# Kernel optimization log

Hardware: AMD Instinct MI355X
Metric: run time of the kernel (lower is better)

## Reference

```python
import jax, jax.numpy as jnp
import numpy as np

NUM_NODES = 50000
NUM_EDGES = 800000
NUM_GRAPHS = 64
EMBED = 128
HIDDEN = 128
LAYERS = 3
CLUSTERS = 16
OUT_DIM = 128
MAX_DEG = 64
EPS = 1e-5


def setup_inputs() -> dict:
    key = jax.random.key(0)
    ks = jax.random.split(key, 16)
    deg_idx = jax.random.randint(ks[0], (NUM_NODES,), 0, MAX_DEG + 1)
    edge_index = jax.random.randint(ks[1], (2, NUM_EDGES), 0, NUM_NODES)
    batch = jnp.sort(jax.random.randint(ks[2], (NUM_NODES,), 0, NUM_GRAPHS))
    s = 0.05
    emb = jax.random.normal(ks[3], (MAX_DEG + 1, EMBED), jnp.float32) * s
    Wl = jax.random.normal(ks[4], (LAYERS, HIDDEN, HIDDEN), jnp.float32) * s
    bl = jnp.zeros((LAYERS, HIDDEN), jnp.float32)
    Wr = jax.random.normal(ks[5], (LAYERS, HIDDEN, HIDDEN), jnp.float32) * s
    gamma = jnp.ones((LAYERS, HIDDEN), jnp.float32)
    beta = jnp.zeros((LAYERS, HIDDEN), jnp.float32)
    attn_W = jax.random.normal(ks[6], (HIDDEN, CLUSTERS), jnp.float32) * s
    attn_b = jnp.zeros((CLUSTERS,), jnp.float32)
    out_W = jax.random.normal(ks[7], (HIDDEN, OUT_DIM), jnp.float32) * s
    out_b = jnp.zeros((OUT_DIM,), jnp.float32)
    return {"emb": emb, "Wl": Wl, "bl": bl, "Wr": Wr, "gamma": gamma,
            "beta": beta, "attn_W": attn_W, "attn_b": attn_b,
            "out_W": out_W, "out_b": out_b, "deg_idx": deg_idx,
            "edge_index": edge_index, "batch": batch}


def reference(emb, Wl, bl, Wr, gamma, beta, attn_W, attn_b, out_W, out_b,
              deg_idx, edge_index, batch):
    N = deg_idx.shape[0]
    src, dst = edge_index[0], edge_index[1]
    x = emb[deg_idx]  # [N, EMBED]
    for l in range(Wl.shape[0]):
        # SAGEConv (mean aggr): lin_l(mean_j x_j) + lin_r(x); lin_r has no bias
        msg_sum = jax.ops.segment_sum(x[src], dst, num_segments=N)
        cnt = jax.ops.segment_sum(jnp.ones((src.shape[0], 1), x.dtype), dst,
                                  num_segments=N)
        mean = msg_sum / jnp.maximum(cnt, 1.0)
        x = mean @ Wl[l] + bl[l] + x @ Wr[l]
        # BatchNorm1d (training-mode batch stats, biased variance)
        mu = x.mean(axis=0)
        var = jnp.mean((x - mu) ** 2, axis=0)
        x = (x - mu) * jax.lax.rsqrt(var + EPS) * gamma[l] + beta[l]
        x = jax.nn.relu(x)  # dropout is identity in eval
    scores = x @ attn_W + attn_b  # [N, C] (num_heads == 1 -> squeeze)
    # per-graph softmax over nodes (segment softmax along dim 0)
    smax = jax.ops.segment_max(scores, batch, num_segments=NUM_GRAPHS)
    e = jnp.exp(scores - smax[batch])
    denom = jax.ops.segment_sum(e, batch, num_segments=NUM_GRAPHS)
    w = e / denom[batch]  # [N, C]
    # c_b = w_b^T @ x_b  -> segment-weighted sums: [B, C, H]
    clust = jax.ops.segment_sum(w[:, :, None] * x[:, None, :], batch,
                                num_segments=NUM_GRAPHS)
    return clust @ out_W + out_b  # [B, C, OUT_DIM]
```

## Files before the change

kernel.cpp:

```cpp
#include <hip/hip_runtime.h>

typedef unsigned short u16;
typedef unsigned int   u32;

#define H    128
#define C    16
#define ODIM 128

typedef short bf16x8 __attribute__((ext_vector_type(8)));
typedef float f32x4  __attribute__((ext_vector_type(4)));

#define WSP 272

__device__ __forceinline__ float bf2f(u32 v){
  union { u32 i; float f; } t; t.i = v << 16; return t.f;
}
__device__ __forceinline__ u16 f2bf(float f){
  u32 u = __float_as_uint(f);
  u32 r = u + 0x7fffu + ((u >> 16) & 1u);
  return (u16)(r >> 16);
}
__device__ __forceinline__ u32 pack2(float a, float b){
  return (u32)f2bf(a) | ((u32)f2bf(b) << 16);
}

__global__ __launch_bounds__(256) void k_embed(const float* __restrict__ emb,
    const int* __restrict__ deg, u16* __restrict__ xb, int N){
  int i = blockIdx.x*256 + threadIdx.x;
  if (i >= N*32) return;
  int n = i >> 5, q = i & 31;
  int d = deg[n];
  float4 v = ((const float4*)(emb + (size_t)d*H))[q];
  uint2 o; o.x = pack2(v.x, v.y); o.y = pack2(v.z, v.w);
  ((uint2*)(xb + (size_t)n*H))[q] = o;
}

__global__ __launch_bounds__(256) void k_bounds(const int* __restrict__ batch,
    int* __restrict__ gs, int N, int B){
  int n = blockIdx.x*256 + threadIdx.x;
  if (n >= N) return;
  int b = batch[n];
  if (n == 0){ for (int g = 0; g <= b; g++) gs[g] = 0; }
  else {
    int pb = batch[n-1];
    for (int g = pb+1; g <= b; g++) gs[g] = n;
  }
  if (n == N-1){ for (int g = b+1; g <= B; g++) gs[g] = N; }
}

__global__ __launch_bounds__(256) void k_wprep(const float* __restrict__ Wl,
    const float* __restrict__ Wr, u16* __restrict__ Wt){
  __shared__ u16 T[128][18];
  int b = blockIdx.x;
  int strip = b & 7, half = (b >> 3) & 1, l = b >> 4;
  const float* M = (half ? Wr : Wl) + (size_t)l*H*H;
  int k0 = strip * 16;
  int tid = threadIdx.x;
  #pragma unroll
  for (int j = 0; j < 8; j++){
    int u = tid + j*256;
    int kk = u >> 7, h = u & 127;
    T[h][kk] = f2bf(M[(size_t)(k0 + kk)*H + h]);
  }
  __syncthreads();
  #pragma unroll
  for (int j = 0; j < 8; j++){
    int u = tid + j*256;
    int h = u >> 4, k16 = u & 15;
    Wt[((size_t)(l*H + h))*256 + half*128 + k0 + k16] = T[h][k16];
  }
}


__global__ __launch_bounds__(256) void k_hist(const int* __restrict__ ei,
    int* __restrict__ blkhist, int NB, int E, int chunk){
  __shared__ int hist[400];
  int blk = blockIdx.x, tid = threadIdx.x;
  for (int b = tid; b < NB; b += 256) hist[b] = 0;
  __syncthreads();
  int start = blk*chunk, end = min(E, start + chunk);
  for (int e = start + tid; e < end; e += 256)
    atomicAdd(&hist[ei[E + e] >> 7], 1);
  __syncthreads();
  for (int b = tid; b < NB; b += 256) blkhist[b*64 + blk] = hist[b];
}

__global__ __launch_bounds__(256) void k_scanA(const int* __restrict__ in,
    int* __restrict__ out, int* __restrict__ bsum, int n){
  __shared__ int wsum[4];
  int tid = threadIdx.x;
  int base = blockIdx.x*1024 + tid*4;
  int v0 = (base+0 < n) ? in[base+0] : 0;
  int v1 = (base+1 < n) ? in[base+1] : 0;
  int v2 = (base+2 < n) ? in[base+2] : 0;
  int v3 = (base+3 < n) ? in[base+3] : 0;
  int tsum = v0+v1+v2+v3;
  int lane = tid & 63, w = tid >> 6;
  int incl = tsum;
  for (int d = 1; d < 64; d <<= 1){
    int t = __shfl_up(incl, d, 64);
    if (lane >= d) incl += t;
  }
  if (lane == 63) wsum[w] = incl;
  __syncthreads();
  int woff = 0;
  for (int i = 0; i < w; i++) woff += wsum[i];
  int excl = woff + incl - tsum;
  if (base+0 < n) out[base+0] = excl;
  if (base+1 < n) out[base+1] = excl + v0;
  if (base+2 < n) out[base+2] = excl + v0 + v1;
  if (base+3 < n) out[base+3] = excl + v0 + v1 + v2;
  if (tid == 255) bsum[blockIdx.x] = woff + incl;
}

__global__ __launch_bounds__(64) void k_scanB(const int* __restrict__ bsum,
    int* __restrict__ boff, int nb){
  int tid = threadIdx.x;
  int v = (tid < nb) ? bsum[tid] : 0;
  int incl = v;
  for (int d = 1; d < 64; d <<= 1){
    int t = __shfl_up(incl, d, 64);
    if (tid >= d) incl += t;
  }
  boff[tid] = incl - v;
}

__global__ __launch_bounds__(256) void k_scanC(int* __restrict__ out,
    const int* __restrict__ boff, int n){
  int i = blockIdx.x*256 + threadIdx.x;
  if (i < n) out[i] += boff[i >> 10];
}

__global__ __launch_bounds__(256) void k_place(const int* __restrict__ ei,
    const int* __restrict__ bases, int2* __restrict__ pairs,
    int NB, int E, int chunk){
  __shared__ int cursor[400];
  int blk = blockIdx.x, tid = threadIdx.x;
  for (int b = tid; b < NB; b += 256) cursor[b] = bases[b*64 + blk];
  __syncthreads();
  int start = blk*chunk, end = min(E, start + chunk);
  for (int e = start + tid; e < end; e += 256){
    int s = ei[e], d = ei[E + e];
    int pos = atomicAdd(&cursor[d >> 7], 1);
    pairs[pos] = make_int2(s, d);
  }
}

__global__ __launch_bounds__(256) void k_cnt_place(const int2* __restrict__ pairs,
    const int* __restrict__ bases, int* __restrict__ rowptr,
    int* __restrict__ col, int NB, int N, int E){
  int b = blockIdx.x, tid = threadIdx.x;
  int bstart = bases[b*64];
  int bend   = (b+1 < NB) ? bases[(b+1)*64] : E;
  __shared__ int cnt[128], sc[128], rank[128];
  if (tid < 128) cnt[tid] = 0;
  __syncthreads();
  for (int e = bstart + tid; e < bend; e += 256)
    atomicAdd(&cnt[pairs[e].y & 127], 1);
  __syncthreads();
  if (tid < 128) sc[tid] = cnt[tid];
  for (int d = 1; d < 128; d <<= 1){
    int v = 0;
    __syncthreads();
    if (tid < 128 && tid >= d) v = sc[tid - d];
    __syncthreads();
    if (tid < 128) sc[tid] += v;
  }
  __syncthreads();
  if (tid < 128){
    int excl = sc[tid] - cnt[tid];
    rank[tid] = bstart + excl;
    int node = b*128 + tid;
    if (node < N) rowptr[node] = bstart + excl;
  }
  if (b == NB-1 && tid == 0) rowptr[N] = E;
  __syncthreads();
  for (int e = bstart + tid; e < bend; e += 256){
    int2 p = pairs[e];
    int pos = atomicAdd(&rank[p.y & 127], 1);
    col[pos] = p.x;
  }
}

__global__ __launch_bounds__(256) void k_agg(const u16* __restrict__ x,
    const int* __restrict__ rowptr, const int* __restrict__ col,
    u16* __restrict__ meanb, int N){
  int wid  = (blockIdx.x*256 + threadIdx.x) >> 6;
  int lane = threadIdx.x & 63;
  if (wid >= N) return;
  int r0 = rowptr[wid], r1 = rowptr[wid+1];
  int grp = lane >> 4, fl = lane & 15;
  const u16* xf = x + fl*8;
  float a0=0.f,a1=0.f,a2=0.f,a3=0.f,a4=0.f,a5=0.f,a6=0.f,a7=0.f;
  for (int e = r0 + grp; e < r1; e += 4){
    int s = col[e];
    uint4 v = *(const uint4*)(xf + (size_t)s*H);
    a0 += bf2f(v.x & 0xffff); a1 += bf2f(v.x >> 16);
    a2 += bf2f(v.y & 0xffff); a3 += bf2f(v.y >> 16);
    a4 += bf2f(v.z & 0xffff); a5 += bf2f(v.z >> 16);
    a6 += bf2f(v.w & 0xffff); a7 += bf2f(v.w >> 16);
  }
  a0 += __shfl_xor(a0,16,64); a1 += __shfl_xor(a1,16,64);
  a2 += __shfl_xor(a2,16,64); a3 += __shfl_xor(a3,16,64);
  a4 += __shfl_xor(a4,16,64); a5 += __shfl_xor(a5,16,64);
  a6 += __shfl_xor(a6,16,64); a7 += __shfl_xor(a7,16,64);
  a0 += __shfl_xor(a0,32,64); a1 += __shfl_xor(a1,32,64);
  a2 += __shfl_xor(a2,32,64); a3 += __shfl_xor(a3,32,64);
  a4 += __shfl_xor(a4,32,64); a5 += __shfl_xor(a5,32,64);
  a6 += __shfl_xor(a6,32,64); a7 += __shfl_xor(a7,32,64);
  if (grp == 0){
    float invc = 1.0f / (float)max(r1 - r0, 1);
    uint4 o;
    o.x = pack2(a0*invc, a1*invc);
    o.y = pack2(a2*invc, a3*invc);
    o.z = pack2(a4*invc, a5*invc);
    o.w = pack2(a6*invc, a7*invc);
    *(uint4*)(meanb + (size_t)wid*H + fl*8) = o;
  }
}

__global__ __launch_bounds__(256) void k_linear(const u16* __restrict__ meanb,
    const u16* __restrict__ xb, const u16* __restrict__ Wt,
    const float* __restrict__ bl, float* __restrict__ x2,
    float* __restrict__ pstats, int N){
  __shared__ u16 Ws[128][WSP];
  __shared__ float Sh[128], Qh[128];
  int tid = threadIdx.x;
  if (tid < 128){ Sh[tid] = 0.f; Qh[tid] = 0.f; }
  int lane = tid & 63, w = tid >> 6;
  int mlane = lane & 15, quad = lane >> 4;
  int node = blockIdx.x*64 + w*16 + mlane;
  const u16* arow_m = meanb + (size_t)node*H + quad*8;
  const u16* arow_x = xb   + (size_t)node*H + quad*8;
  bf16x8 af[8];
  #pragma unroll
  for (int kk = 0; kk < 4; kk++){
    af[kk]     = *(const bf16x8*)(arow_m + kk*32);
    af[kk + 4] = *(const bf16x8*)(arow_x + kk*32);
  }
  #pragma unroll
  for (int j = 0; j < 16; j++){
    int u = tid + j*256;
    int row = u >> 5, seg = u & 31;
    uint4 v = ((const uint4*)(Wt + (size_t)row*256))[seg];
    *(uint4*)&Ws[row][seg*8] = v;
  }
  __syncthreads();
  f32x4 acc[8];
  #pragma unroll
  for (int t = 0; t < 8; t++) acc[t] = (f32x4){0.f, 0.f, 0.f, 0.f};
  #pragma unroll
  for (int kk = 0; kk < 8; kk++){
    #pragma unroll
    for (int t = 0; t < 8; t++){
      bf16x8 b = *(const bf16x8*)&Ws[t*16 + mlane][kk*32 + quad*8];
      acc[t] = __builtin_amdgcn_mfma_f32_16x16x32_bf16(af[kk], b, acc[t], 0, 0, 0);
    }
  }
  #pragma unroll
  for (int t = 0; t < 8; t++){
    int h = t*16 + mlane;
    float bv = bl[h];
    float s = 0.f, q = 0.f;
    #pragma unroll
    for (int r = 0; r < 4; r++){
      int nd = blockIdx.x*64 + w*16 + quad*4 + r;
      if (nd < N){
        float v = acc[t][r] + bv;
        x2[(size_t)nd*H + h] = v;
        s += v; q = fmaf(v, v, q);
      }
    }
    s += __shfl_xor(s, 16, 64); s += __shfl_xor(s, 32, 64);
    q += __shfl_xor(q, 16, 64); q += __shfl_xor(q, 32, 64);
    if (quad == 0){
      atomicAdd(&Sh[h], s);
      atomicAdd(&Qh[h], q);
    }
  }
  __syncthreads();
  {
    float v = (tid < 128) ? Sh[tid] : Qh[tid - 128];
    pstats[(size_t)blockIdx.x*256 + tid] = v;
  }
}

__global__ __launch_bounds__(256) void k_statred(const float* __restrict__ pstats,
    float* __restrict__ stats, int nblk){
  __shared__ float red[4];
  int c = blockIdx.x, tid = threadIdx.x;
  float s = 0.f;
  for (int b = tid; b < nblk; b += 256)
    s += pstats[(size_t)b*256 + c];
  s += __shfl_xor(s, 1, 64);  s += __shfl_xor(s, 2, 64);
  s += __shfl_xor(s, 4, 64);  s += __shfl_xor(s, 8, 64);
  s += __shfl_xor(s, 16, 64); s += __shfl_xor(s, 32, 64);
  if ((tid & 63) == 0) red[tid >> 6] = s;
  __syncthreads();
  if (tid == 0) stats[c] = red[0] + red[1] + red[2] + red[3];
}

__global__ __launch_bounds__(256) void k_bnrelu(const float* __restrict__ x2,
    const float* __restrict__ stats, const float* __restrict__ gamma,
    const float* __restrict__ beta, u16* __restrict__ xb, int N, float invN){
  int i = blockIdx.x*256 + threadIdx.x;
  if (i >= N*32) return;
  int h = (i & 31) * 4;
  float4 v = ((const float4*)x2)[i];
  float vv[4] = {v.x, v.y, v.z, v.w};
  float r[4];
  #pragma unroll
  for (int j = 0; j < 4; j++){
    float mu  = stats[h+j] * invN;
    float var = fmaf(-mu, mu, stats[H + h + j] * invN);
    float sc  = rsqrtf(var + 1e-5f) * gamma[h+j];
    float bi  = beta[h+j];
    r[j] = fmaxf(fmaf(vv[j] - mu, sc, bi), 0.0f);
  }
  uint2 o; o.x = pack2(r[0], r[1]); o.y = pack2(r[2], r[3]);
  ((uint2*)xb)[i] = o;
}

__global__ __launch_bounds__(256) void k_scores(const u16* __restrict__ xb,
    const float* __restrict__ attn_W, const float* __restrict__ attn_b,
    float* __restrict__ escore, int N){
  __shared__ float xs[64][133];
  __shared__ float aw[H*C];
  int tid = threadIdx.x;
  int n0 = blockIdx.x * 64;
  #pragma unroll
  for (int j = 0; j < 8; j++){
    int u = tid + j*256;
    aw[u] = attn_W[u];
  }
  #pragma unroll
  for (int j = 0; j < 4; j++){
    int u = tid + j*256;
    int row = u & 63, seg = u >> 6;
    int node = n0 + row;
    uint4 rv = make_uint4(0,0,0,0);
    if (node < N) rv = ((const uint4*)(xb + (size_t)node*H))[seg];
    int k = seg*8;
    xs[row][k+0]=bf2f(rv.x&0xffff); xs[row][k+1]=bf2f(rv.x>>16);
    xs[row][k+2]=bf2f(rv.y&0xffff); xs[row][k+3]=bf2f(rv.y>>16);
    xs[row][k+4]=bf2f(rv.z&0xffff); xs[row][k+5]=bf2f(rv.z>>16);
    xs[row][k+6]=bf2f(rv.w&0xffff); xs[row][k+7]=bf2f(rv.w>>16);
  }
  __syncthreads();
  int c = tid & 15, sub = tid >> 4;
  float bias = attn_b[c];
  float acc[4] = {bias, bias, bias, bias};
  for (int k = 0; k < H; k++){
    float w = aw[k*C + c];
    acc[0] = fmaf(xs[sub     ][k], w, acc[0]);
    acc[1] = fmaf(xs[sub + 16][k], w, acc[1]);
    acc[2] = fmaf(xs[sub + 32][k], w, acc[2]);
    acc[3] = fmaf(xs[sub + 48][k], w, acc[3]);
  }
  #pragma unroll
  for (int j = 0; j < 4; j++){
    int node = n0 + sub + 16*j;
    if (node < N) escore[(size_t)node*C + c] = __expf(acc[j]);
  }
}

__global__ __launch_bounds__(256) void k_denom(const float* __restrict__ escore,
    const int* __restrict__ gs, float* __restrict__ gsum){
  int g = blockIdx.x;
  int c = threadIdx.x & 15, sub = threadIdx.x >> 4;
  int a = gs[g], b = gs[g+1];
  float s = 0.f;
  for (int n = a + sub; n < b; n += 16) s += escore[(size_t)n*C + c];
  __shared__ float part[16][17];
  part[sub][c] = s;
  for (int off2 = 8; off2 > 0; off2 >>= 1){
    __syncthreads();
    if (sub < off2) part[sub][c] += part[sub + off2][c];
  }
  __syncthreads();
  if (threadIdx.x < C) gsum[(size_t)g*C + threadIdx.x] = part[0][threadIdx.x];
}

__global__ __launch_bounds__(256) void k_clust(const u16* __restrict__ xb,
    const float* __restrict__ escore, const int* __restrict__ gs,
    float* __restrict__ partial){
  int g = blockIdx.x >> 4, b = blockIdx.x & 15;
  int h = threadIdx.x & 127, cg = threadIdx.x >> 7;
  int a = gs[g], e2 = gs[g+1];
  float acc[8] = {0,0,0,0,0,0,0,0};
  for (int n = a + b; n < e2; n += 16){
    float xv = bf2f(xb[(size_t)n*H + h]);
    const float4* ep = (const float4*)(escore + (size_t)n*C) + cg*2;
    float4 e0 = ep[0], e1 = ep[1];
    acc[0] = fmaf(e0.x, xv, acc[0]);
    acc[1] = fmaf(e0.y, xv, acc[1]);
    acc[2] = fmaf(e0.z, xv, acc[2]);
    acc[3] = fmaf(e0.w, xv, acc[3]);
    acc[4] = fmaf(e1.x, xv, acc[4]);
    acc[5] = fmaf(e1.y, xv, acc[5]);
    acc[6] = fmaf(e1.z, xv, acc[6]);
    acc[7] = fmaf(e1.w, xv, acc[7]);
  }
  int c0 = cg*8;
  float* dst = partial + (((size_t)(g*16 + b))*C)*H + h;
  #pragma unroll
  for (int r = 0; r < 8; r++)
    dst[(size_t)(c0 + r)*H] = acc[r];
}

__global__ __launch_bounds__(256) void k_out(const float* __restrict__ partial,
    const float* __restrict__ gsum, const float* __restrict__ out_W,
    const float* __restrict__ out_b, float* __restrict__ out){
  __shared__ float cs[2][128];
  int tid = threadIdx.x;
  int r = tid >> 7, h = tid & 127;
  int row = blockIdx.x*2 + r;
  int g = row >> 4, c = row & 15;
  float s = 0.f;
  for (int b = 0; b < 16; b++)
    s += partial[(((size_t)(g*16 + b))*C + c)*H + h];
  cs[r][h] = s;
  __syncthreads();
  float gden = gsum[row];
  float inv = gden > 0.f ? 1.0f / gden : 0.f;
  float acc = 0.f;
  for (int hh = 0; hh < H; hh++)
    acc = fmaf(cs[r][hh], out_W[hh*ODIM + h], acc);
  out[(size_t)row*ODIM + h] = fmaf(acc, inv, out_b[h]);
}

extern "C" void kernel_launch(void* const* d_in, const int* in_sizes, int n_in,
                              void* d_out, int out_size, void* d_ws, size_t ws_size,
                              hipStream_t stream){
  const float* emb    = (const float*)d_in[0];
  const float* Wl     = (const float*)d_in[1];
  const float* bl     = (const float*)d_in[2];
  const float* Wr     = (const float*)d_in[3];
  const float* gamma  = (const float*)d_in[4];
  const float* beta   = (const float*)d_in[5];
  const float* attn_W = (const float*)d_in[6];
  const float* attn_b = (const float*)d_in[7];
  const float* out_W  = (const float*)d_in[8];
  const float* out_b  = (const float*)d_in[9];
  const int* deg    = (const int*)d_in[10];
  const int* ei     = (const int*)d_in[11];
  const int* batch  = (const int*)d_in[12];
  float* out = (float*)d_out;

  const int N = in_sizes[10];
  const int E = in_sizes[11] / 2;
  const int L = in_sizes[1] / (H*H);
  const int B = out_size / (C*ODIM);
  const int NB = (N + 127) >> 7;
  const int n25 = NB * 64;
  const int chunk = (E + 63) >> 6;
  const int nblkL = (N + 63) / 64;

  size_t off = 0;
  auto alloc = [&](size_t bytes) -> void* {
    void* p = (char*)d_ws + off;
    off += (bytes + 255) & ~(size_t)255;
    return p;
  };
  u16*   xb     = (u16*)  alloc((size_t)N*H*2);
  u16*   meanb  = (u16*)  alloc((size_t)N*H*2);
  float* x2     = (float*)alloc((size_t)N*H*4);
  int2*  pairs  = (int2*)x2;
  float* partial= x2;
  u16*   Wt     = (u16*)  alloc((size_t)L*H*256*2);
  float* escore = (float*)alloc((size_t)N*C*4);
  int*   col    = (int*)  alloc((size_t)E*4);
  int*   rowptr = (int*)  alloc((size_t)(N+1)*4);
  int*   blkhist= (int*)  alloc((size_t)n25*4);
  int*   bases  = (int*)  alloc((size_t)n25*4);
  int*   bsum   = (int*)  alloc(64*4);
  int*   boff   = (int*)  alloc(64*4);
  int*   gs     = (int*)  alloc((size_t)(B+1)*4);
  float* gsum   = (float*)alloc((size_t)B*C*4);
  float* stats  = (float*)alloc((size_t)L*2*H*4);
  float* pstats = (float*)alloc((size_t)nblkL*256*4);

  hipLaunchKernelGGL(k_embed,  dim3((N*32+255)/256), dim3(256), 0, stream, emb, deg, xb, N);
  hipLaunchKernelGGL(k_bounds, dim3((N+255)/256),    dim3(256), 0, stream, batch, gs, N, B);
  hipLaunchKernelGGL(k_wprep,  dim3(L*16),           dim3(256), 0, stream, Wl, Wr, Wt);
  hipLaunchKernelGGL(k_hist,   dim3(64),  dim3(256), 0, stream, ei, blkhist, NB, E, chunk);
  int nblk25 = (n25 + 1023) / 1024;
  hipLaunchKernelGGL(k_scanA,  dim3(nblk25), dim3(256), 0, stream, blkhist, bases, bsum, n25);
  hipLaunchKernelGGL(k_scanB,  dim3(1),      dim3(64),  0, stream, bsum, boff, nblk25);
  hipLaunchKernelGGL(k_scanC,  dim3((n25+255)/256), dim3(256), 0, stream, bases, boff, n25);
  hipLaunchKernelGGL(k_place,  dim3(64),  dim3(256), 0, stream, ei, bases, pairs, NB, E, chunk);
  hipLaunchKernelGGL(k_cnt_place, dim3(NB), dim3(256), 0, stream, pairs, bases, rowptr, col, NB, N, E);

  float invN = 1.0f / (float)N;
  for (int l = 0; l < L; l++){
    hipLaunchKernelGGL(k_agg,    dim3((N+3)/4),  dim3(256), 0, stream, xb, rowptr, col, meanb, N);
    hipLaunchKernelGGL(k_linear, dim3(nblkL),    dim3(256), 0, stream,
                       meanb, xb, Wt + (size_t)l*H*256, bl + (size_t)l*H, x2,
                       pstats, N);
    hipLaunchKernelGGL(k_statred,dim3(256),      dim3(256), 0, stream, pstats, stats + l*2*H, nblkL);
    hipLaunchKernelGGL(k_bnrelu, dim3((N*32+255)/256), dim3(256), 0, stream,
                       x2, stats + l*2*H, gamma + (size_t)l*H, beta + (size_t)l*H, xb, N, invN);
  }
  hipLaunchKernelGGL(k_scores, dim3((N+63)/64), dim3(256), 0, stream, xb, attn_W, attn_b, escore, N);
  hipLaunchKernelGGL(k_denom,  dim3(B),         dim3(256), 0, stream, escore, gs, gsum);
  hipLaunchKernelGGL(k_clust,  dim3(B*16),      dim3(256), 0, stream, xb, escore, gs, partial);
  hipLaunchKernelGGL(k_out,    dim3(B*C/2),     dim3(256), 0, stream, partial, gsum, out_W, out_b, out);
}
```

Baseline: 396.4 us.

## Fuse setup kernels, widen edge binning, unroll gather, fuse scores into BN

Merges the embed, graph-bounds, weight-prep and histogram kernels into a single block-partitioned setup launch. The edge binning now uses 256 chunks instead of 64 for more parallelism, with the scan widened to match. The aggregation loop is unrolled by two to keep more gathers in flight. The attention score computation is folded into the final BN/ReLU pass so the last-layer activations are not re-read. Together these cut launch count and memory traffic, at the cost of a larger histogram and extra shared memory and a block-wide barrier in the BN kernel.

```diff
diff --git a/kernel.cpp b/kernel.cpp
--- a/kernel.cpp
+++ b/kernel.cpp
@@ -11,6 +11,7 @@
 typedef float f32x4  __attribute__((ext_vector_type(4)));
 
 #define WSP 272
+#define NP  256
 
 __device__ __forceinline__ float bf2f(u32 v){
   union { u32 i; float f; } t; t.i = v << 16; return t.f;
@@ -24,65 +25,65 @@
   return (u32)f2bf(a) | ((u32)f2bf(b) << 16);
 }
 
-__global__ __launch_bounds__(256) void k_embed(const float* __restrict__ emb,
-    const int* __restrict__ deg, u16* __restrict__ xb, int N){
-  int i = blockIdx.x*256 + threadIdx.x;
-  if (i >= N*32) return;
-  int n = i >> 5, q = i & 31;
-  int d = deg[n];
-  float4 v = ((const float4*)(emb + (size_t)d*H))[q];
-  uint2 o; o.x = pack2(v.x, v.y); o.y = pack2(v.z, v.w);
-  ((uint2*)(xb + (size_t)n*H))[q] = o;
-}
-
-__global__ __launch_bounds__(256) void k_bounds(const int* __restrict__ batch,
-    int* __restrict__ gs, int N, int B){
-  int n = blockIdx.x*256 + threadIdx.x;
-  if (n >= N) return;
-  int b = batch[n];
-  if (n == 0){ for (int g = 0; g <= b; g++) gs[g] = 0; }
-  else {
-    int pb = batch[n-1];
-    for (int g = pb+1; g <= b; g++) gs[g] = n;
-  }
-  if (n == N-1){ for (int g = b+1; g <= B; g++) gs[g] = N; }
-}
-
-__global__ __launch_bounds__(256) void k_wprep(const float* __restrict__ Wl,
-    const float* __restrict__ Wr, u16* __restrict__ Wt){
-  __shared__ u16 T[128][18];
-  int b = blockIdx.x;
-  int strip = b & 7, half = (b >> 3) & 1, l = b >> 4;
-  const float* M = (half ? Wr : Wl) + (size_t)l*H*H;
-  int k0 = strip * 16;
-  int tid = threadIdx.x;
-  #pragma unroll
-  for (int j = 0; j < 8; j++){
-    int u = tid + j*256;
-    int kk = u >> 7, h = u & 127;
-    T[h][kk] = f2bf(M[(size_t)(k0 + kk)*H + h]);
-  }
-  __syncthreads();
-  #pragma unroll
-  for (int j = 0; j < 8; j++){
-    int u = tid + j*256;
-    int h = u >> 4, k16 = u & 15;
-    Wt[((size_t)(l*H + h))*256 + half*128 + k0 + k16] = T[h][k16];
-  }
-}
-
-
-__global__ __launch_bounds__(256) void k_hist(const int* __restrict__ ei,
-    int* __restrict__ blkhist, int NB, int E, int chunk){
-  __shared__ int hist[400];
-  int blk = blockIdx.x, tid = threadIdx.x;
-  for (int b = tid; b < NB; b += 256) hist[b] = 0;
-  __syncthreads();
-  int start = blk*chunk, end = min(E, start + chunk);
-  for (int e = start + tid; e < end; e += 256)
-    atomicAdd(&hist[ei[E + e] >> 7], 1);
-  __syncthreads();
-  for (int b = tid; b < NB; b += 256) blkhist[b*64 + blk] = hist[b];
+__global__ __launch_bounds__(256) void k_setup(const float* __restrict__ emb,
+    const int* __restrict__ deg, u16* __restrict__ xb,
+    const int* __restrict__ batch, int* __restrict__ gs,
+    const float* __restrict__ Wl, const float* __restrict__ Wr,
+    u16* __restrict__ Wt, const int* __restrict__ ei,
+    int* __restrict__ blkhist, int N, int B, int NB, int E, int chunk,
+    int g0, int g1, int g2){
+  __shared__ __align__(16) char smem[4608];
+  int bid = blockIdx.x, tid = threadIdx.x;
+  if (bid < g0){
+    int i = bid*256 + tid;
+    if (i < N*32){
+      int n = i >> 5, q = i & 31;
+      int d = deg[n];
+      float4 v = ((const float4*)(emb + (size_t)d*H))[q];
+      uint2 o; o.x = pack2(v.x, v.y); o.y = pack2(v.z, v.w);
+      ((uint2*)(xb + (size_t)n*H))[q] = o;
+    }
+  } else if (bid < g1){
+    int n = (bid - g0)*256 + tid;
+    if (n < N){
+      int b = batch[n];
+      if (n == 0){ for (int g = 0; g <= b; g++) gs[g] = 0; }
+      else {
+        int pb = batch[n-1];
+        for (int g = pb+1; g <= b; g++) gs[g] = n;
+      }
+      if (n == N-1){ for (int g = b+1; g <= B; g++) gs[g] = N; }
+    }
+  } else if (bid < g2){
+    u16 (*T)[18] = (u16(*)[18])smem;
+    int b = bid - g1;
+    int strip = b & 7, half = (b >> 3) & 1, l = b >> 4;
+    const float* M = (half ? Wr : Wl) + (size_t)l*H*H;
+    int k0 = strip * 16;
+    #pragma unroll
+    for (int j = 0; j < 8; j++){
+      int u = tid + j*256;
+      int kk = u >> 7, h = u & 127;
+      T[h][kk] = f2bf(M[(size_t)(k0 + kk)*H + h]);
+    }
+    __syncthreads();
+    #pragma unroll
+    for (int j = 0; j < 8; j++){
+      int u = tid + j*256;
+      int h = u >> 4, k16 = u & 15;
+      Wt[((size_t)(l*H + h))*256 + half*128 + k0 + k16] = T[h][k16];
+    }
+  } else {
+    int* hist = (int*)smem;
+    int blk = bid - g2;
+    for (int b = tid; b < NB; b += 256) hist[b] = 0;
+    __syncthreads();
+    int start = blk*chunk, end = min(E, start + chunk);
+    for (int e = start + tid; e < end; e += 256)
+      atomicAdd(&hist[ei[E + e] >> 7], 1);
+    __syncthreads();
+    for (int b = tid; b < NB; b += 256) blkhist[b*NP + blk] = hist[b];
+  }
 }
 
 __global__ __launch_bounds__(256) void k_scanA(const int* __restrict__ in,
@@ -113,16 +114,22 @@
   if (tid == 255) bsum[blockIdx.x] = woff + incl;
 }
 
-__global__ __launch_bounds__(64) void k_scanB(const int* __restrict__ bsum,
+__global__ __launch_bounds__(256) void k_scanB(const int* __restrict__ bsum,
     int* __restrict__ boff, int nb){
+  __shared__ int ws[4];
   int tid = threadIdx.x;
   int v = (tid < nb) ? bsum[tid] : 0;
+  int lane = tid & 63, w = tid >> 6;
   int incl = v;
   for (int d = 1; d < 64; d <<= 1){
     int t = __shfl_up(incl, d, 64);
-    if (tid >= d) incl += t;
-  }
-  boff[tid] = incl - v;
+    if (lane >= d) incl += t;
+  }
+  if (lane == 63) ws[w] = incl;
+  __syncthreads();
+  int woff = 0;
+  for (int i = 0; i < w; i++) woff += ws[i];
+  boff[tid] = woff + incl - v;
 }
 
 __global__ __launch_bounds__(256) void k_scanC(int* __restrict__ out,
@@ -136,7 +143,7 @@
     int NB, int E, int chunk){
   __shared__ int cursor[400];
   int blk = blockIdx.x, tid = threadIdx.x;
-  for (int b = tid; b < NB; b += 256) cursor[b] = bases[b*64 + blk];
+  for (int b = tid; b < NB; b += 256) cursor[b] = bases[b*NP + blk];
   __syncthreads();
   int start = blk*chunk, end = min(E, start + chunk);
   for (int e = start + tid; e < end; e += 256){
@@ -150,8 +157,8 @@
     const int* __restrict__ bases, int* __restrict__ rowptr,
     int* __restrict__ col, int NB, int N, int E){
   int b = blockIdx.x, tid = threadIdx.x;
-  int bstart = bases[b*64];
-  int bend   = (b+1 < NB) ? bases[(b+1)*64] : E;
+  int bstart = bases[b*NP];
+  int bend   = (b+1 < NB) ? bases[(b+1)*NP] : E;
   __shared__ int cnt[128], sc[128], rank[128];
   if (tid < 128) cnt[tid] = 0;
   __syncthreads();
@@ -192,9 +199,22 @@
   int grp = lane >> 4, fl = lane & 15;
   const u16* xf = x + fl*8;
   float a0=0.f,a1=0.f,a2=0.f,a3=0.f,a4=0.f,a5=0.f,a6=0.f,a7=0.f;
-  for (int e = r0 + grp; e < r1; e += 4){
-    int s = col[e];
-    uint4 v = *(const uint4*)(xf + (size_t)s*H);
+  int e = r0 + grp;
+  for (; e + 4 < r1; e += 8){
+    int s0 = col[e], s1 = col[e+4];
+    uint4 v = *(const uint4*)(xf + (size_t)s0*H);
+    uint4 u = *(const uint4*)(xf + (size_t)s1*H);
+    a0 += bf2f(v.x & 0xffff) + bf2f(u.x & 0xffff);
+    a1 += bf2f(v.x >> 16)    + bf2f(u.x >> 16);
+    a2 += bf2f(v.y & 0xffff) + bf2f(u.y & 0xffff);
+    a3 += bf2f(v.y >> 16)    + bf2f(u.y >> 16);
+    a4 += bf2f(v.z & 0xffff) + bf2f(u.z & 0xffff);
+    a5 += bf2f(v.z >> 16)    + bf2f(u.z >> 16);
+    a6 += bf2f(v.w & 0xffff) + bf2f(u.w & 0xffff);
+    a7 += bf2f(v.w >> 16)    + bf2f(u.w >> 16);
+  }
+  if (e < r1){
+    uint4 v = *(const uint4*)(xf + (size_t)col[e]*H);
     a0 += bf2f(v.x & 0xffff); a1 += bf2f(v.x >> 16);
     a2 += bf2f(v.y & 0xffff); a3 += bf2f(v.y >> 16);
     a4 += bf2f(v.z & 0xffff); a5 += bf2f(v.z >> 16);
@@ -302,65 +322,51 @@
 
 __global__ __launch_bounds__(256) void k_bnrelu(const float* __restrict__ x2,
     const float* __restrict__ stats, const float* __restrict__ gamma,
-    const float* __restrict__ beta, u16* __restrict__ xb, int N, float invN){
-  int i = blockIdx.x*256 + threadIdx.x;
-  if (i >= N*32) return;
-  int h = (i & 31) * 4;
-  float4 v = ((const float4*)x2)[i];
-  float vv[4] = {v.x, v.y, v.z, v.w};
-  float r[4];
-  #pragma unroll
-  for (int j = 0; j < 4; j++){
-    float mu  = stats[h+j] * invN;
-    float var = fmaf(-mu, mu, stats[H + h + j] * invN);
-    float sc  = rsqrtf(var + 1e-5f) * gamma[h+j];
-    float bi  = beta[h+j];
-    r[j] = fmaxf(fmaf(vv[j] - mu, sc, bi), 0.0f);
-  }
-  uint2 o; o.x = pack2(r[0], r[1]); o.y = pack2(r[2], r[3]);
-  ((uint2*)xb)[i] = o;
-}
-
-__global__ __launch_bounds__(256) void k_scores(const u16* __restrict__ xb,
+    const float* __restrict__ beta, u16* __restrict__ xb, int N, float invN,
     const float* __restrict__ attn_W, const float* __restrict__ attn_b,
-    float* __restrict__ escore, int N){
-  __shared__ float xs[64][133];
+    float* __restrict__ escore, int do_scores){
+  __shared__ float xs[8][132];
   __shared__ float aw[H*C];
+  __shared__ float ab[C];
   int tid = threadIdx.x;
-  int n0 = blockIdx.x * 64;
-  #pragma unroll
-  for (int j = 0; j < 8; j++){
-    int u = tid + j*256;
-    aw[u] = attn_W[u];
-  }
-  #pragma unroll
-  for (int j = 0; j < 4; j++){
-    int u = tid + j*256;
-    int row = u & 63, seg = u >> 6;
-    int node = n0 + row;
-    uint4 rv = make_uint4(0,0,0,0);
-    if (node < N) rv = ((const uint4*)(xb + (size_t)node*H))[seg];
-    int k = seg*8;
-    xs[row][k+0]=bf2f(rv.x&0xffff); xs[row][k+1]=bf2f(rv.x>>16);
-    xs[row][k+2]=bf2f(rv.y&0xffff); xs[row][k+3]=bf2f(rv.y>>16);
-    xs[row][k+4]=bf2f(rv.z&0xffff); xs[row][k+5]=bf2f(rv.z>>16);
-    xs[row][k+6]=bf2f(rv.w&0xffff); xs[row][k+7]=bf2f(rv.w>>16);
-  }
-  __syncthreads();
-  int c = tid & 15, sub = tid >> 4;
-  float bias = attn_b[c];
-  float acc[4] = {bias, bias, bias, bias};
-  for (int k = 0; k < H; k++){
-    float w = aw[k*C + c];
-    acc[0] = fmaf(xs[sub     ][k], w, acc[0]);
-    acc[1] = fmaf(xs[sub + 16][k], w, acc[1]);
-    acc[2] = fmaf(xs[sub + 32][k], w, acc[2]);
-    acc[3] = fmaf(xs[sub + 48][k], w, acc[3]);
-  }
-  #pragma unroll
-  for (int j = 0; j < 4; j++){
-    int node = n0 + sub + 16*j;
-    if (node < N) escore[(size_t)node*C + c] = __expf(acc[j]);
+  int i = blockIdx.x*256 + tid;
+  bool active = (i < N*32);
+  int h = (tid & 31) * 4;
+  float r[4] = {0.f, 0.f, 0.f, 0.f};
+  if (active){
+    float4 v = ((const float4*)x2)[i];
+    float vv[4] = {v.x, v.y, v.z, v.w};
+    #pragma unroll
+    for (int j = 0; j < 4; j++){
+      float mu  = stats[h+j] * invN;
+      float var = fmaf(-mu, mu, stats[H + h + j] * invN);
+      float sc  = rsqrtf(var + 1e-5f) * gamma[h+j];
+      float bi  = beta[h+j];
+      r[j] = fmaxf(fmaf(vv[j] - mu, sc, bi), 0.0f);
+    }
+    uint2 o; o.x = pack2(r[0], r[1]); o.y = pack2(r[2], r[3]);
+    ((uint2*)xb)[i] = o;
+  }
+  if (do_scores){
+    #pragma unroll
+    for (int j = 0; j < 8; j++) aw[tid + j*256] = attn_W[tid + j*256];
+    if (tid < C) ab[tid] = attn_b[tid];
+    int ln = tid >> 5;
+    if (active){
+      xs[ln][h+0]=r[0]; xs[ln][h+1]=r[1]; xs[ln][h+2]=r[2]; xs[ln][h+3]=r[3];
+    }
+    __syncthreads();
+    if (tid < 128){
+      int n2 = tid >> 4, c = tid & 15;
+      int node = blockIdx.x*8 + n2;
+      if (node < N){
+        float acc = ab[c];
+        #pragma unroll 4
+        for (int k = 0; k < H; k++)
+          acc = fmaf(xs[n2][k], aw[k*C + c], acc);
+        escore[(size_t)node*C + c] = __expf(acc);
+      }
+    }
   }
 }
 
@@ -452,8 +458,8 @@
   const int L = in_sizes[1] / (H*H);
   const int B = out_size / (C*ODIM);
   const int NB = (N + 127) >> 7;
-  const int n25 = NB * 64;
-  const int chunk = (E + 63) >> 6;
+  const int nbh = NB * NP;
+  const int chunk = (E + NP - 1) / NP;
   const int nblkL = (N + 63) / 64;
 
   size_t off = 0;
@@ -471,24 +477,27 @@
   float* escore = (float*)alloc((size_t)N*C*4);
   int*   col    = (int*)  alloc((size_t)E*4);
   int*   rowptr = (int*)  alloc((size_t)(N+1)*4);
-  int*   blkhist= (int*)  alloc((size_t)n25*4);
-  int*   bases  = (int*)  alloc((size_t)n25*4);
-  int*   bsum   = (int*)  alloc(64*4);
-  int*   boff   = (int*)  alloc(64*4);
+  int*   blkhist= (int*)  alloc((size_t)nbh*4);
+  int*   bases  = (int*)  alloc((size_t)nbh*4);
+  int*   bsum   = (int*)  alloc(256*4);
+  int*   boff   = (int*)  alloc(256*4);
   int*   gs     = (int*)  alloc((size_t)(B+1)*4);
   float* gsum   = (float*)alloc((size_t)B*C*4);
   float* stats  = (float*)alloc((size_t)L*2*H*4);
   float* pstats = (float*)alloc((size_t)nblkL*256*4);
 
-  hipLaunchKernelGGL(k_embed,  dim3((N*32+255)/256), dim3(256), 0, stream, emb, deg, xb, N);
-  hipLaunchKernelGGL(k_bounds, dim3((N+255)/256),    dim3(256), 0, stream, batch, gs, N, B);
-  hipLaunchKernelGGL(k_wprep,  dim3(L*16),           dim3(256), 0, stream, Wl, Wr, Wt);
-  hipLaunchKernelGGL(k_hist,   dim3(64),  dim3(256), 0, stream, ei, blkhist, NB, E, chunk);
-  int nblk25 = (n25 + 1023) / 1024;
-  hipLaunchKernelGGL(k_scanA,  dim3(nblk25), dim3(256), 0, stream, blkhist, bases, bsum, n25);
-  hipLaunchKernelGGL(k_scanB,  dim3(1),      dim3(64),  0, stream, bsum, boff, nblk25);
-  hipLaunchKernelGGL(k_scanC,  dim3((n25+255)/256), dim3(256), 0, stream, bases, boff, n25);
-  hipLaunchKernelGGL(k_place,  dim3(64),  dim3(256), 0, stream, ei, bases, pairs, NB, E, chunk);
+  int g0 = (N*32 + 255)/256;
+  int g1 = g0 + (N + 255)/256;
+  int g2 = g1 + L*16;
+  int gT = g2 + NP;
+  hipLaunchKernelGGL(k_setup, dim3(gT), dim3(256), 0, stream,
+                     emb, deg, xb, batch, gs, Wl, Wr, Wt, ei, blkhist,
+                     N, B, NB, E, chunk, g0, g1, g2);
+  int nblkS = (nbh + 1023) / 1024;
+  hipLaunchKernelGGL(k_scanA,  dim3(nblkS), dim3(256), 0, stream, blkhist, bases, bsum, nbh);
+  hipLaunchKernelGGL(k_scanB,  dim3(1),     dim3(256), 0, stream, bsum, boff, nblkS);
+  hipLaunchKernelGGL(k_scanC,  dim3((nbh+255)/256), dim3(256), 0, stream, bases, boff, nbh);
+  hipLaunchKernelGGL(k_place,  dim3(NP), dim3(256), 0, stream, ei, bases, pairs, NB, E, chunk);
   hipLaunchKernelGGL(k_cnt_place, dim3(NB), dim3(256), 0, stream, pairs, bases, rowptr, col, NB, N, E);
 
   float invN = 1.0f / (float)N;
@@ -499,10 +508,10 @@
                        pstats, N);
     hipLaunchKernelGGL(k_statred,dim3(256),      dim3(256), 0, stream, pstats, stats + l*2*H, nblkL);
     hipLaunchKernelGGL(k_bnrelu, dim3((N*32+255)/256), dim3(256), 0, stream,
-                       x2, stats + l*2*H, gamma + (size_t)l*H, beta + (size_t)l*H, xb, N, invN);
-  }
-  hipLaunchKernelGGL(k_scores, dim3((N+63)/64), dim3(256), 0, stream, xb, attn_W, attn_b, escore, N);
-  hipLaunchKernelGGL(k_denom,  dim3(B),         dim3(256), 0, stream, escore, gs, gsum);
-  hipLaunchKernelGGL(k_clust,  dim3(B*16),      dim3(256), 0, stream, xb, escore, gs, partial);
-  hipLaunchKernelGGL(k_out,    dim3(B*C/2),     dim3(256), 0, stream, partial, gsum, out_W, out_b, out);
-}
+                       x2, stats + l*2*H, gamma + (size_t)l*H, beta + (size_t)l*H,
+                       xb, N, invN, attn_W, attn_b, escore, (l == L-1) ? 1 : 0);
+  }
+  hipLaunchKernelGGL(k_denom,  dim3(B),     dim3(256), 0, stream, escore, gs, gsum);
+  hipLaunchKernelGGL(k_clust,  dim3(B*16),  dim3(256), 0, stream, xb, escore, gs, partial);
+  hipLaunchKernelGGL(k_out,    dim3(B*C/2), dim3(256), 0, stream, partial, gsum, out_W, out_b, out);
+}
```

New measurement: 347.7 us. 12.3% less time.
